# Optimization experiments

Measured on AMD Instinct MI355X. Metric: run time of the kernel, lower is better.

Reference implementation:

```python
import jax, jax.numpy as jnp
import numpy as np

B, N, D = 4, 1024, 1024
H = 16
RS, RC = 32, 32
MLP = int(D * 4.0)
EPS = 1e-6


def _ln(x):
    # LayerNorm with no scale/bias (flax defaults: eps=1e-6)
    m = jnp.mean(x, axis=-1, keepdims=True)
    v = jnp.mean(jnp.square(x - m), axis=-1, keepdims=True)
    return (x - m) * jax.lax.rsqrt(v + EPS)


def _rms(x, scale):
    rms = jnp.sqrt(jnp.mean(jnp.square(x), axis=-1, keepdims=True) + EPS)
    return scale * x / rms


def _modulate(x, shift, scale):
    return x * (1 + scale[:, None]) + shift[:, None]


def setup_inputs() -> dict:
    key = jax.random.key(0)
    ks = jax.random.split(key, 20)
    s = 0.02
    return {
        'x': jax.random.normal(ks[0], (B, N, D), jnp.float32),
        'c': jax.random.normal(ks[1], (B, D), jnp.float32),
        'cls_token': jax.random.normal(ks[2], (B, D), jnp.float32),
        'Wc': jax.random.normal(ks[3], (D, 6 * D), jnp.float32) * s,
        'bc': jax.random.normal(ks[4], (6 * D,), jnp.float32) * s,
        'Wqkv': jax.random.normal(ks[5], (D, 3 * D), jnp.float32) * s,
        'bqkv': jnp.zeros((3 * D,), jnp.float32),
        'Wo': jax.random.normal(ks[6], (D, D), jnp.float32) * s,
        'bo': jnp.zeros((D,), jnp.float32),
        'A_s': jax.random.normal(ks[7], (D, RS), jnp.float32) * s,
        'B_s': jax.random.normal(ks[8], (RS, D), jnp.float32) * s,
        'rms_s_scale': jnp.ones((D,), jnp.float32),
        'C_r': jax.random.normal(ks[9], (D, RC), jnp.float32) * s,
        'D_r': jax.random.normal(ks[10], (RC, D), jnp.float32) * s,
        'rms_c_scale': jnp.ones((D,), jnp.float32),
        'W1': jax.random.normal(ks[11], (D, MLP), jnp.float32) * s,
        'b1': jnp.zeros((MLP,), jnp.float32),
        'W2': jax.random.normal(ks[12], (MLP, D), jnp.float32) * s,
        'b2': jnp.zeros((D,), jnp.float32),
    }


def reference(x, c, cls_token, Wc, bc, Wqkv, bqkv, Wo, bo, A_s, B_s,
              rms_s_scale, C_r, D_r, rms_c_scale, W1, b1, W2, b2):
    hd = D // H
    # AdaLN conditioning
    c_proj = jax.nn.silu(c) @ Wc + bc                    # (B, 6D)
    shift_a, scale_a, gate_a, shift_m, scale_m, gate_m = jnp.split(c_proj, 6, axis=-1)

    # Self-attention branch
    x_norm = _modulate(_ln(x), shift_a, scale_a)         # (B, N, D)
    qkv = x_norm @ Wqkv + bqkv                           # (B, N, 3D)
    q, k, v = jnp.split(qkv, 3, axis=-1)
    q = q.reshape(B, N, H, hd).transpose(0, 2, 1, 3)     # (B, H, N, hd)
    k = k.reshape(B, N, H, hd).transpose(0, 2, 1, 3)
    v = v.reshape(B, N, H, hd).transpose(0, 2, 1, 3)
    attn_w = jax.nn.softmax(jnp.einsum('bhqd,bhkd->bhqk', q, k) * hd ** (-0.5), axis=-1)
    attn_out = jnp.einsum('bhqk,bhkd->bhqd', attn_w, v)
    attn_out = attn_out.transpose(0, 2, 1, 3).reshape(B, N, D)
    attn_out = attn_out @ Wo + bo
    Y = x + gate_a[:, None] * attn_out

    # Self-gram low-rank branch (residual)
    gram_s = (x @ A_s) @ B_s                             # (B, N, D)
    X_prime = _rms(gram_s, rms_s_scale) + Y

    # Cross-gram branch via CLS token (no residual)
    u_c = cls_token[:, :, None] * C_r[None]              # (B, D, RC)
    v_c = jnp.einsum('bnd,bdr->bnr', X_prime, u_c)       # (B, N, RC)
    gram_c = v_c @ D_r                                   # (B, N, D)
    Z = _rms(gram_c, rms_c_scale)

    # MLP branch
    z_norm = _modulate(_ln(Z), shift_m, scale_m)
    h = jax.nn.gelu(z_norm @ W1 + b1) @ W2 + b2
    return Z + gate_m[:, None] * h
```

## Files before the change

### kernel.cpp

```cpp
#include <hip/hip_runtime.h>
#include <stdint.h>

typedef float  f32x4  __attribute__((ext_vector_type(4)));
typedef int    i32x4  __attribute__((ext_vector_type(4)));
typedef __bf16 bf16x4 __attribute__((ext_vector_type(4)));

#define D_    1024
#define SIXD  6144
#define QSCALE 0.18033688011112042f

#define BAR() asm volatile("s_barrier" ::: "memory")

__device__ __forceinline__ void mfma16(const i32x4 &a, const i32x4 &b, f32x4 &c) {
  asm("v_mfma_f32_16x16x32_bf16 %0, %1, %2, %0" : "+v"(c) : "v"(a), "v"(b));
}
__device__ __forceinline__ void mfma16a(const i32x4 &a, const i32x4 &b, f32x4 &c) {
  asm("v_mfma_f32_16x16x32_bf16 %0, %1, %2, %0" : "+a"(c) : "v"(a), "v"(b));
}

__device__ __forceinline__ void gload_lds16(const void* g, void* l) {
  __builtin_amdgcn_global_load_lds(
      (const __attribute__((address_space(1))) uint32_t*)g,
      (__attribute__((address_space(3))) uint32_t*)l, 16, 0, 0);
}

__global__ __launch_bounds__(256)
void cond_gemm(const float* __restrict__ c, const float* __restrict__ Wc,
               const float* __restrict__ bc, float* __restrict__ cproj)
{
  __shared__ float sc[4096];
  __shared__ float tp[8][4][32];
  int tid = threadIdx.x;
  for (int i = tid; i < 4096; i += 256) {
    float v = c[i];
    sc[i] = v / (1.f + __expf(-v));
  }
  __syncthreads();
  int colo = tid & 31, kseg = tid >> 5;
  int col = blockIdx.x * 32 + colo;
  float a0 = 0.f, a1 = 0.f, a2 = 0.f, a3 = 0.f;
  for (int k = kseg * 128; k < kseg * 128 + 128; k++) {
    float w = Wc[(size_t)k * SIXD + col];
    a0 += sc[k] * w; a1 += sc[1024 + k] * w;
    a2 += sc[2048 + k] * w; a3 += sc[3072 + k] * w;
  }
  tp[kseg][0][colo] = a0; tp[kseg][1][colo] = a1;
  tp[kseg][2][colo] = a2; tp[kseg][3][colo] = a3;
  __syncthreads();
  if (kseg == 0) {
#pragma unroll
    for (int b = 0; b < 4; b++) {
      float s = bc[col];
#pragma unroll
      for (int g = 0; g < 8; g++) s += tp[g][b][colo];
      cproj[b * SIXD + col] = s;
    }
  }
}

__global__ __launch_bounds__(256)
void transpose_all(const float* __restrict__ Wqkv, const float* __restrict__ Wo,
                   const float* __restrict__ W1, const float* __restrict__ W2,
                   __bf16* __restrict__ Wqkvt, __bf16* __restrict__ Wot,
                   __bf16* __restrict__ W1t, __bf16* __restrict__ W2t)
{
  __shared__ __bf16 t[64][65];
  int bid = blockIdx.x;
  const float* W; __bf16* Wt; int Kdim, Ndim, lb;
  if (bid < 768)       { W = Wqkv; Wt = Wqkvt; Kdim = 1024; Ndim = 3072; lb = bid; }
  else if (bid < 1024) { W = Wo;   Wt = Wot;   Kdim = 1024; Ndim = 1024; lb = bid - 768; }
  else if (bid < 2048) { W = W1;   Wt = W1t;   Kdim = 1024; Ndim = 4096; lb = bid - 1024; }
  else                 { W = W2;   Wt = W2t;   Kdim = 4096; Ndim = 1024; lb = bid - 2048; }
  int ntn = Ndim >> 6;
  int kt = lb / ntn, nt = lb % ntn;
  int tid = threadIdx.x;
  const float* src = W + (size_t)(kt * 64) * Ndim + nt * 64;
#pragma unroll
  for (int i = 0; i < 4; i++) {
    int k = i * 16 + (tid >> 4);
    int c4 = tid & 15;
    float4 v = ((const float4*)(src + (size_t)k * Ndim))[c4];
    t[k][c4 * 4 + 0] = (__bf16)v.x; t[k][c4 * 4 + 1] = (__bf16)v.y;
    t[k][c4 * 4 + 2] = (__bf16)v.z; t[k][c4 * 4 + 3] = (__bf16)v.w;
  }
  __syncthreads();
  __bf16* dst = Wt + (size_t)(nt * 64) * Kdim + kt * 64;
  int n = tid >> 2, ks = (tid & 3) * 16;
  bf16x4 o0, o1, o2, o3;
#pragma unroll
  for (int j = 0; j < 4; j++) {
    o0[j] = t[ks + j][n];      o1[j] = t[ks + 4 + j][n];
    o2[j] = t[ks + 8 + j][n];  o3[j] = t[ks + 12 + j][n];
  }
  __bf16* dp = dst + (size_t)n * Kdim + ks;
  *(bf16x4*)(dp) = o0; *(bf16x4*)(dp + 4) = o1;
  *(bf16x4*)(dp + 8) = o2; *(bf16x4*)(dp + 12) = o3;
}

__global__ __launch_bounds__(256)
void transpose_v(const __bf16* __restrict__ qkv, __bf16* __restrict__ Vt)
{
  __shared__ __bf16 t[32][33];
  int bid = blockIdx.x;
  int dt = bid & 1, nt = (bid >> 1) & 31, bh = bid >> 6;
  int b = bh >> 4, h = bh & 15;
  int x = threadIdx.x & 31, yq = threadIdx.x >> 5;
  const __bf16* src = qkv + ((size_t)(b * 1024 + nt * 32)) * 3072 + 2048 + h * 64 + dt * 32;
#pragma unroll
  for (int i = 0; i < 4; i++) {
    int row = yq * 4 + i;
    t[row][x] = src[(size_t)row * 3072 + x];
  }
  __syncthreads();
  __bf16* dst = Vt + ((size_t)(bh * 64 + dt * 32)) * 1024 + nt * 32;
#pragma unroll
  for (int i = 0; i < 4; i++) {
    int drow = yq * 4 + i;
    dst[(size_t)drow * 1024 + x] = t[x][drow];
  }
}

__global__ __launch_bounds__(256)
void ln_mod(const float* __restrict__ X, const float* __restrict__ cproj,
            int shift_off, int scale_off, __bf16* __restrict__ Out)
{
  int row = blockIdx.x;
  int b = row >> 10;
  int tid = threadIdx.x;
  const float4* xr = (const float4*)(X + (size_t)row * D_);
  float4 v = xr[tid];
  float s  = v.x + v.y + v.z + v.w;
  float s2 = v.x * v.x + v.y * v.y + v.z * v.z + v.w * v.w;
#pragma unroll
  for (int off = 1; off < 64; off <<= 1) {
    s  += __shfl_xor(s,  off, 64);
    s2 += __shfl_xor(s2, off, 64);
  }
  __shared__ float red[8];
  int wave = tid >> 6, lane = tid & 63;
  if (lane == 0) { red[wave] = s; red[4 + wave] = s2; }
  __syncthreads();
  s  = red[0] + red[1] + red[2] + red[3];
  s2 = red[4] + red[5] + red[6] + red[7];
  float mean = s * (1.f / D_);
  float var  = s2 * (1.f / D_) - mean * mean;
  float rstd = rsqrtf(var + 1e-6f);
  const float4* sh = (const float4*)(cproj + b * SIXD + shift_off);
  const float4* sc = (const float4*)(cproj + b * SIXD + scale_off);
  float4 shv = sh[tid], scv = sc[tid];
  bf16x4 o;
  o[0] = (__bf16)((v.x - mean) * rstd * (1.f + scv.x) + shv.x);
  o[1] = (__bf16)((v.y - mean) * rstd * (1.f + scv.y) + shv.y);
  o[2] = (__bf16)((v.z - mean) * rstd * (1.f + scv.z) + shv.z);
  o[3] = (__bf16)((v.w - mean) * rstd * (1.f + scv.w) + shv.w);
  *(bf16x4*)(Out + (size_t)row * D_ + tid * 4) = o;
}

template<int EPI, int NBUF>
__global__ __launch_bounds__(256)
void gemm_bt(const __bf16* __restrict__ A, const __bf16* __restrict__ Bt,
             const float* __restrict__ bias, const float* __restrict__ cproj,
             int gate_off, const float* __restrict__ resid,
             void* __restrict__ Cout, void* __restrict__ Cout2,
             void* __restrict__ Cout3, void* __restrict__ Cout4,
             int M, int N, int K, int SK)
{
  __shared__ __align__(16) __bf16 As[NBUF * 128 * 32];
  __shared__ __align__(16) __bf16 Bs[NBUF * 128 * 32];
  const int PD = NBUF - 1;
  int tilesN = N >> 7, tilesM = M >> 7;
  int npersk = tilesM * tilesN;
  int sk = blockIdx.x / npersk;
  int rest = blockIdx.x % npersk;
  int cpx = npersk >> 3;
  rest = (rest & 7) * cpx + (rest >> 3);
  int bm = rest / tilesN, bn = rest % tilesN;
  int Klen = K / SK, Kstart = sk * Klen;

  int tid = threadIdx.x;
  int lane = tid & 63, wave = tid >> 6;
  int lr = lane & 15, lg = lane >> 4;
  int wm = (wave >> 1) << 6, wn = (wave & 1) << 6;

  f32x4 acc[4][4] = {};

  int sr = tid >> 2, skb = tid & 3;
  int scol = ((skb ^ ((sr >> 1) & 3)) * 8);
  const __bf16* pa = A + (size_t)((bm << 7) + sr) * K + Kstart + scol;
  const __bf16* pb = Bt + (size_t)((bn << 7) + sr) * K + Kstart + scol;
  const size_t rstep = (size_t)64 * K;
  __bf16* la = As + tid * 8;
  __bf16* lb = Bs + tid * 8;

  auto STAGE = [&](int buf, int k0) {
    int bo = buf * 4096;
    gload_lds16(pa + k0, la + bo);
    gload_lds16(pa + rstep + k0, la + bo + 2048);
    gload_lds16(pb + k0, lb + bo);
    gload_lds16(pb + rstep + k0, lb + bo + 2048);
  };

  int nt = Klen >> 5;
#pragma unroll
  for (int p = 0; p < PD; p++) STAGE(p, p * 32);

  for (int t = 0; t < nt; t++) {
    if (t + PD < nt) STAGE((t + PD) % NBUF, (t + PD) * 32);
    int ahead = nt - 1 - t; if (ahead > PD) ahead = PD;
    if (ahead >= 3)      asm volatile("s_waitcnt vmcnt(12)" ::: "memory");
    else if (ahead == 2) asm volatile("s_waitcnt vmcnt(8)" ::: "memory");
    else if (ahead == 1) asm volatile("s_waitcnt vmcnt(4)" ::: "memory");
    else                 asm volatile("s_waitcnt vmcnt(0)" ::: "memory");
    BAR();
    const __bf16* Ac = As + (t % NBUF) * 4096;
    const __bf16* Bc = Bs + (t % NBUF) * 4096;
    i32x4 af[4], bfv[4];
#pragma unroll
    for (int m = 0; m < 4; m++) {
      int row = wm + m * 16 + lr;
      af[m] = *(const i32x4*)(Ac + row * 32 + ((lg ^ ((row >> 1) & 3)) * 8));
    }
#pragma unroll
    for (int n = 0; n < 4; n++) {
      int row = wn + n * 16 + lr;
      bfv[n] = *(const i32x4*)(Bc + row * 32 + ((lg ^ ((row >> 1) & 3)) * 8));
    }
    asm volatile("s_waitcnt lgkmcnt(0)" ::: "memory");
    __builtin_amdgcn_sched_barrier(0);
    BAR();
    __builtin_amdgcn_s_setprio(1);
#pragma unroll
    for (int m = 0; m < 4; m++)
#pragma unroll
      for (int n = 0; n < 4; n++)
        mfma16(af[m], bfv[n], acc[m][n]);
    __builtin_amdgcn_s_setprio(0);
  }
  asm volatile("s_waitcnt vmcnt(0)" ::: "memory");
  asm volatile("s_nop 7\n\ts_nop 7" ::);

  __bf16* Pp = nullptr;
  if (EPI == 3) {
    if (sk == 0)      Pp = (__bf16*)Cout;
    else if (sk == 1) Pp = (__bf16*)Cout2;
    else if (sk == 2) Pp = (__bf16*)Cout3;
    else              Pp = (__bf16*)Cout4;
  }

  int row0 = (bm << 7) + wm;
  int col0 = (bn << 7) + wn;
#pragma unroll
  for (int m = 0; m < 4; m++) {
#pragma unroll
    for (int n = 0; n < 4; n++) {
      int cc = col0 + n * 16 + lr;
      float bv = (EPI == 3) ? 0.f : bias[cc];
#pragma unroll
      for (int r = 0; r < 4; r++) {
        int row = row0 + m * 16 + (lg << 2) + r;
        float v = acc[m][n][r] + bv;
        size_t idx = (size_t)row * N + cc;
        if (EPI == 0) {
          ((__bf16*)Cout)[idx] = (__bf16)v;
        } else if (EPI == 1) {
          int b = row >> 10;
          float g = cproj[b * SIXD + gate_off + cc];
          ((float*)Cout)[idx] = resid[idx] + g * v;
        } else if (EPI == 2) {
          float u = 0.7978845608028654f * (v + 0.044715f * v * v * v);
          u = fminf(fmaxf(u, -15.f), 15.f);
          float e = __expf(2.f * u);
          float th = (e - 1.f) / (e + 1.f);
          ((__bf16*)Cout)[idx] = (__bf16)(0.5f * v * (1.f + th));
        } else if (EPI == 4) {
          float scq = (cc < 1024) ? QSCALE : 1.f;
          ((__bf16*)Cout)[idx] = (__bf16)(v * scq);
        } else {
          Pp[idx] = (__bf16)v;
        }
      }
    }
  }
}

template<int EPI, int NT, int KD>
__global__ __launch_bounds__(512, 2)
void gemm256(const __bf16* __restrict__ A, const __bf16* __restrict__ Bt,
             const float* __restrict__ bias,
             void* __restrict__ Cout, void* __restrict__ Cout2,
             void* __restrict__ Cout3, void* __restrict__ Cout4,
             int M, int N)
{
  __shared__ __align__(16) __bf16 As[2 * 16384];
  __shared__ __align__(16) __bf16 Bs[2 * 16384];
  int tilesN = N >> 8, tilesM = M >> 8;
  int npersk = tilesM * tilesN;
  int sk = blockIdx.x / npersk;
  int rest = blockIdx.x % npersk;
  int cpx = npersk >> 3;
  rest = (rest & 7) * cpx + (rest >> 3);
  int bm = rest / tilesN, bn = rest % tilesN;
  int Kstart = sk * (NT * 64);

  int tid = threadIdx.x;
  int lane = tid & 63, wave = tid >> 6;
  int lr = lane & 15, lg = lane >> 4;
  int wr = wave >> 2, wc = wave & 3;

  f32x4 acc[8][4] = {};

  int srow = tid >> 3;
  int schunk = (tid & 7) ^ (srow & 7);
  const __bf16* pa = A  + (size_t)((bm << 8) + srow) * KD + Kstart + schunk * 8;
  const __bf16* pb = Bt + (size_t)((bn << 8) + srow) * KD + Kstart + schunk * 8;
  __bf16* la = As + tid * 8;
  __bf16* lb = Bs + tid * 8;

  gload_lds16(pa,                 la);
  gload_lds16(pa + 64 * KD,       la + 4096);
  gload_lds16(pa + 128 * KD,      la + 8192);
  gload_lds16(pa + 192 * KD,      la + 12288);
  gload_lds16(pb,                 lb);
  gload_lds16(pb + 64 * KD,       lb + 4096);
  gload_lds16(pb + 128 * KD,      lb + 8192);
  gload_lds16(pb + 192 * KD,      lb + 12288);
  gload_lds16(pb + 64,            lb + 16384);
  gload_lds16(pb + 64 * KD + 64,  lb + 16384 + 4096);
  gload_lds16(pb + 128 * KD + 64, lb + 16384 + 8192);
  gload_lds16(pb + 192 * KD + 64, lb + 16384 + 12288);
  asm volatile("s_waitcnt vmcnt(4)" ::: "memory");
  BAR();

  int cc0 = ((lg ^ (lr & 7)) << 4);
  int cc1 = cc0 ^ 64;
  const char* aA = (const char*)As + (wr * 128 + lr) * 128;
  const char* aB = (const char*)Bs + (wc * 64 + lr) * 128;

  i32x4 alo[4][2], ahi[4][2], b0v[2][2], b1v[2][2];
#pragma unroll
  for (int m = 0; m < 4; m++) {
    alo[m][0] = *(const i32x4*)(aA + m * 2048 + cc0);
    alo[m][1] = *(const i32x4*)(aA + m * 2048 + cc1);
  }
#pragma unroll
  for (int n = 0; n < 2; n++) {
    b0v[n][0] = *(const i32x4*)(aB + n * 2048 + cc0);
    b0v[n][1] = *(const i32x4*)(aB + n * 2048 + cc1);
  }

  for (int t = 0; t < NT; t++) {
    const char* Ab = aA + (t & 1) * 32768;
    const char* Bb = aB + (t & 1) * 32768;
    int nb = ((t + 1) & 1) * 16384;
    int ob = (t & 1) * 16384;

#pragma unroll
    for (int n = 0; n < 2; n++) {
      b1v[n][0] = *(const i32x4*)(Bb + 4096 + n * 2048 + cc0);
      b1v[n][1] = *(const i32x4*)(Bb + 4096 + n * 2048 + cc1);
    }
    if (t + 1 < NT) {
      gload_lds16(pa + 64,            la + nb);
      gload_lds16(pa + 128 * KD + 64, la + nb + 8192);
    }
    __builtin_amdgcn_s_setprio(1);
#pragma unroll
    for (int m = 0; m < 4; m++)
#pragma unroll
      for (int n = 0; n < 2; n++) {
        mfma16a(alo[m][0], b0v[n][0], acc[m][n]);
        mfma16a(alo[m][1], b0v[n][1], acc[m][n]);
      }
    __builtin_amdgcn_s_setprio(0);
    BAR();

#pragma unroll
    for (int m = 0; m < 4; m++) {
      ahi[m][0] = *(const i32x4*)(Ab + 8192 + m * 2048 + cc0);
      ahi[m][1] = *(const i32x4*)(Ab + 8192 + m * 2048 + cc1);
    }
    if (t + 1 < NT) {
      gload_lds16(pa + 64 * KD + 64,  la + nb + 4096);
      gload_lds16(pa + 192 * KD + 64, la + nb + 12288);
    }
    __builtin_amdgcn_s_setprio(1);
#pragma unroll
    for (int m = 0; m < 4; m++)
#pragma unroll
      for (int n = 0; n < 2; n++) {
        mfma16a(alo[m][0], b1v[n][0], acc[m][2 + n]);
        mfma16a(alo[m][1], b1v[n][1], acc[m][2 + n]);
      }
    __builtin_amdgcn_s_setprio(0);
    BAR();

    if (t + 2 < NT) {
      gload_lds16(pb + 128,           lb + ob);
      gload_lds16(pb + 64 * KD + 128, lb + ob + 4096);
    }
    __builtin_amdgcn_s_setprio(1);
#pragma unroll
    for (int m = 0; m < 4; m++)
#pragma unroll
      for (int n = 0; n < 2; n++) {
        mfma16a(ahi[m][0], b1v[n][0], acc[4 + m][2 + n]);
        mfma16a(ahi[m][1], b1v[n][1], acc[4 + m][2 + n]);
      }
    __builtin_amdgcn_s_setprio(0);
    if (t + 1 < NT) {
      if (t + 2 < NT) asm volatile("s_waitcnt vmcnt(2)" ::: "memory");
      else            asm volatile("s_waitcnt vmcnt(0)" ::: "memory");
    }
    BAR();

    if (t + 2 < NT) {
      gload_lds16(pb + 128 * KD + 128, lb + ob + 8192);
      gload_lds16(pb + 192 * KD + 128, lb + ob + 12288);
    }
    __builtin_amdgcn_s_setprio(1);
#pragma unroll
    for (int m = 0; m < 4; m++)
#pragma unroll
      for (int n = 0; n < 2; n++) {
        mfma16a(ahi[m][0], b0v[n][0], acc[4 + m][n]);
        mfma16a(ahi[m][1], b0v[n][1], acc[4 + m][n]);
      }
    __builtin_amdgcn_s_setprio(0);
    if (t + 1 < NT) {
      const char* An = aA + ((t + 1) & 1) * 32768;
      const char* Bn = aB + ((t + 1) & 1) * 32768;
#pragma unroll
      for (int m = 0; m < 4; m++) {
        alo[m][0] = *(const i32x4*)(An + m * 2048 + cc0);
        alo[m][1] = *(const i32x4*)(An + m * 2048 + cc1);
      }
#pragma unroll
      for (int n = 0; n < 2; n++) {
        b0v[n][0] = *(const i32x4*)(Bn + n * 2048 + cc0);
        b0v[n][1] = *(const i32x4*)(Bn + n * 2048 + cc1);
      }
    }
    BAR();
    pa += 64; pb += 64;
  }
  asm volatile("s_nop 7\n\ts_nop 7" ::);

  __bf16* Pp = nullptr;
  if (EPI == 3) {
    if (sk == 0)      Pp = (__bf16*)Cout;
    else if (sk == 1) Pp = (__bf16*)Cout2;
    else if (sk == 2) Pp = (__bf16*)Cout3;
    else              Pp = (__bf16*)Cout4;
  }

  int row0 = (bm << 8) + wr * 128;
  int col0 = (bn << 8) + wc * 64;
#pragma unroll
  for (int m = 0; m < 8; m++) {
#pragma unroll
    for (int n = 0; n < 4; n++) {
      int cc = col0 + n * 16 + lr;
      float bv = (EPI == 3) ? 0.f : bias[cc];
#pragma unroll
      for (int r = 0; r < 4; r++) {
        int row = row0 + m * 16 + (lg << 2) + r;
        float v = acc[m][n][r] + bv;
        size_t idx = (size_t)row * N + cc;
        if (EPI == 2) {
          float u = 0.7978845608028654f * (v + 0.044715f * v * v * v);
          u = fminf(fmaxf(u, -15.f), 15.f);
          float e = __expf(2.f * u);
          float th = (e - 1.f) / (e + 1.f);
          ((__bf16*)Cout)[idx] = (__bf16)(0.5f * v * (1.f + th));
        } else if (EPI == 4) {
          float scq = (cc < 1024) ? QSCALE : 1.f;
          ((__bf16*)Cout)[idx] = (__bf16)(v * scq);
        } else {
          Pp[idx] = (__bf16)v;
        }
      }
    }
  }
}

__global__ __launch_bounds__(256)
void reduce_w2(const __bf16* __restrict__ P0, const __bf16* __restrict__ P1,
               const __bf16* __restrict__ P2, const __bf16* __restrict__ P3,
               const float* __restrict__ bias, const float* __restrict__ cproj,
               float* __restrict__ Out)
{
  int row = blockIdx.x;
  int b = row >> 10;
  int tid = threadIdx.x;
  size_t base = (size_t)row * D_ + tid * 4;
  bf16x4 a0 = *(const bf16x4*)(P0 + base);
  bf16x4 a1 = *(const bf16x4*)(P1 + base);
  bf16x4 a2 = *(const bf16x4*)(P2 + base);
  bf16x4 a3 = *(const bf16x4*)(P3 + base);
  f32x4 s;
#pragma unroll
  for (int i = 0; i < 4; i++)
    s[i] = ((float)a0[i] + (float)a1[i]) + ((float)a2[i] + (float)a3[i]);
  f32x4 bz = *(const f32x4*)(bias + tid * 4);
  f32x4 g  = *(const f32x4*)(cproj + b * SIXD + 5120 + tid * 4);
  f32x4 z  = *(const f32x4*)(Out + base);
  *(f32x4*)(Out + base) = z + g * (s + bz);
}

__global__ __launch_bounds__(512, 4)
void attn_flash(const __bf16* __restrict__ qkv, const __bf16* __restrict__ Vt,
                __bf16* __restrict__ O)
{
  __shared__ __align__(16) __bf16 Kl[2][64 * 64];
  __shared__ __align__(16) __bf16 Vl[2][64 * 64];
  __shared__ __align__(16) __bf16 Pl[8][16 * 64];

  int bid = ((blockIdx.x & 7) << 6) | (blockIdx.x >> 3);
  int qt = bid & 7, h = (bid >> 3) & 15, b = bid >> 7;
  int tid = threadIdx.x, wave = tid >> 6, lane = tid & 63;
  int lr = lane & 15, lg = lane >> 4;

  size_t tok0 = (size_t)b * 1024;
  int qrow = qt * 128 + wave * 16 + lr;
  const __bf16* qptr = qkv + (tok0 + qrow) * 3072 + h * 64;
  i32x4 qf0 = *(const i32x4*)(qptr + lg * 8);
  i32x4 qf1 = *(const i32x4*)(qptr + 32 + lg * 8);

  float l_acc[4] = {0.f, 0.f, 0.f, 0.f};
  f32x4 oacc[4] = {};

  const __bf16* kbase = qkv + tok0 * 3072 + 1024 + h * 64;
  const __bf16* vbase = Vt + ((size_t)(b * 16 + h) * 64) * 1024;

  int skey = tid >> 3, sdb = tid & 7;
  const __bf16* ksrc = kbase + (size_t)skey * 3072 + ((sdb ^ (skey & 7)) * 8);
  const __bf16* vsrc = vbase + (size_t)skey * 1024 + ((sdb ^ (skey & 7)) * 8);
  __bf16* klp = &Kl[0][0] + tid * 8;
  __bf16* vlp = &Vl[0][0] + tid * 8;
  __bf16* pl = &Pl[wave][0];

  auto STAGE = [&](int buf, int kk) {
    gload_lds16(ksrc + (size_t)kk * 3072, klp + buf * 4096);
    gload_lds16(vsrc + kk, vlp + buf * 4096);
  };

  STAGE(0, 0);
  int cur = 0;
  for (int k0 = 0; k0 < 1024; k0 += 64) {
    int kn = (k0 + 64 < 1024) ? (k0 + 64) : k0;
    STAGE(cur ^ 1, kn);
    asm volatile("s_waitcnt vmcnt(2)" ::: "memory");
    BAR();
    const __bf16* K_ = &Kl[cur][0];
    const __bf16* V_ = &Vl[cur][0];

    f32x4 s[4];
    __builtin_amdgcn_s_setprio(1);
#pragma unroll
    for (int n = 0; n < 4; n++) {
      int key = n * 16 + lr;
      int kx = key & 7;
      i32x4 kf0 = *(const i32x4*)(K_ + key * 64 + ((lg ^ kx) * 8));
      i32x4 kf1 = *(const i32x4*)(K_ + key * 64 + (((4 + lg) ^ kx) * 8));
      f32x4 sa = {0.f, 0.f, 0.f, 0.f};
      mfma16(qf0, kf0, sa);
      mfma16(qf1, kf1, sa);
      s[n] = sa;
    }
    __builtin_amdgcn_s_setprio(0);

#pragma unroll
    for (int n = 0; n < 4; n++)
#pragma unroll
      for (int r = 0; r < 4; r++)
        s[n][r] = exp2f(s[n][r]);
#pragma unroll
    for (int r = 0; r < 4; r++)
      l_acc[r] += (s[0][r] + s[1][r]) + (s[2][r] + s[3][r]);

#pragma unroll
    for (int n = 0; n < 4; n++)
#pragma unroll
      for (int r = 0; r < 4; r++) {
        int prow = lg * 4 + r;
        int key = n * 16 + lr;
        int idx = prow * 64 + (((key >> 3) ^ (prow & 7)) * 8) + (key & 7);
        pl[idx] = (__bf16)s[n][r];
      }
    asm volatile("s_waitcnt lgkmcnt(0)" ::: "memory");
    __builtin_amdgcn_sched_barrier(0);
    i32x4 pf0 = *(const i32x4*)(pl + lr * 64 + ((lg ^ (lr & 7)) * 8));
    i32x4 pf1 = *(const i32x4*)(pl + lr * 64 + (((4 + lg) ^ (lr & 7)) * 8));

    __builtin_amdgcn_s_setprio(1);
#pragma unroll
    for (int dt = 0; dt < 4; dt++) {
      int vrow = dt * 16 + lr, rx = vrow & 7;
      i32x4 vf0 = *(const i32x4*)(V_ + vrow * 64 + ((lg ^ rx) * 8));
      i32x4 vf1 = *(const i32x4*)(V_ + vrow * 64 + (((4 + lg) ^ rx) * 8));
      mfma16(pf0, vf0, oacc[dt]);
      mfma16(pf1, vf1, oacc[dt]);
    }
    __builtin_amdgcn_s_setprio(0);
    asm volatile("s_waitcnt lgkmcnt(0)" ::: "memory");
    __builtin_amdgcn_sched_barrier(0);
    BAR();
    cur ^= 1;
  }
  asm volatile("s_waitcnt vmcnt(0)" ::: "memory");
  asm volatile("s_nop 7\n\ts_nop 7" ::);

  float rinv[4];
#pragma unroll
  for (int r = 0; r < 4; r++) {
    float v = l_acc[r];
#pragma unroll
    for (int off = 1; off < 16; off <<= 1) v += __shfl_xor(v, off, 64);
    rinv[r] = 1.f / v;
  }

  int orow = qt * 128 + wave * 16 + (lg << 2);
#pragma unroll
  for (int dt = 0; dt < 4; dt++)
#pragma unroll
    for (int r = 0; r < 4; r++) {
      float v = oacc[dt][r] * rinv[r];
      O[(tok0 + orow + r) * 1024 + h * 64 + dt * 16 + lr] = (__bf16)v;
    }
}

__global__ __launch_bounds__(256)
void gram_fused(const float* __restrict__ X, const float* __restrict__ Y,
                const float* __restrict__ cls,
                const float* __restrict__ A_s, const float* __restrict__ B_s,
                const float* __restrict__ rms_s,
                const float* __restrict__ C_r, const float* __restrict__ D_r,
                const float* __restrict__ rms_c,
                const float* __restrict__ cproj,
                float* __restrict__ Z, __bf16* __restrict__ Znorm)
{
  __shared__ float xs[4][D_];
  __shared__ float tp[8][4][32];
  __shared__ float t1[4][32];
  __shared__ float red[4][4];
  __shared__ float red2[4][4][2];
  int row0 = blockIdx.x * 4;
  int b = row0 >> 10;
  int tid = threadIdx.x;
  int wv = tid >> 6;

  f32x4 cv = *(const f32x4*)(cls + (size_t)b * D_ + tid * 4);
  f32x4 yv[4];
#pragma unroll
  for (int rr = 0; rr < 4; rr++) {
    ((f32x4*)xs[rr])[tid] = *(const f32x4*)(X + (size_t)(row0 + rr) * D_ + tid * 4);
    yv[rr] = *(const f32x4*)(Y + (size_t)(row0 + rr) * D_ + tid * 4);
  }
  __syncthreads();

  {
    int r = tid & 31, seg = tid >> 5;
    float a0 = 0.f, a1 = 0.f, a2 = 0.f, a3 = 0.f;
    const float* ap = A_s + r;
    for (int d = seg * 128; d < seg * 128 + 128; d++) {
      float w = ap[d * 32];
      a0 += xs[0][d] * w; a1 += xs[1][d] * w;
      a2 += xs[2][d] * w; a3 += xs[3][d] * w;
    }
    tp[seg][0][r] = a0; tp[seg][1][r] = a1; tp[seg][2][r] = a2; tp[seg][3][r] = a3;
  }
  __syncthreads();
  if (tid < 128) {
    int rr = tid >> 5, r = tid & 31;
    float sv = 0.f;
#pragma unroll
    for (int g = 0; g < 8; g++) sv += tp[g][rr][r];
    t1[rr][r] = sv;
  }
  __syncthreads();

  f32x4 g[4] = {};
  for (int r = 0; r < 32; r++) {
    f32x4 bv = *(const f32x4*)(B_s + (size_t)r * D_ + tid * 4);
    g[0] += t1[0][r] * bv; g[1] += t1[1][r] * bv;
    g[2] += t1[2][r] * bv; g[3] += t1[3][r] * bv;
  }
  float ssl[4];
#pragma unroll
  for (int rr = 0; rr < 4; rr++)
    ssl[rr] = g[rr][0]*g[rr][0] + g[rr][1]*g[rr][1] + g[rr][2]*g[rr][2] + g[rr][3]*g[rr][3];
#pragma unroll
  for (int off = 1; off < 64; off <<= 1)
#pragma unroll
    for (int rr = 0; rr < 4; rr++) ssl[rr] += __shfl_xor(ssl[rr], off, 64);
  if ((tid & 63) == 0) {
#pragma unroll
    for (int rr = 0; rr < 4; rr++) red[wv][rr] = ssl[rr];
  }
  __syncthreads();
  {
    f32x4 scv = *(const f32x4*)(rms_s + tid * 4);
#pragma unroll
    for (int rr = 0; rr < 4; rr++) {
      float ss = red[0][rr] + red[1][rr] + red[2][rr] + red[3][rr];
      float rs = rsqrtf(ss * (1.f / D_) + 1e-6f);
      f32x4 xp = scv * g[rr] * rs + yv[rr];
      ((f32x4*)xs[rr])[tid] = xp * cv;
    }
  }
  __syncthreads();

  {
    int r = tid & 31, seg = tid >> 5;
    float a0 = 0.f, a1 = 0.f, a2 = 0.f, a3 = 0.f;
    const float* cp = C_r + r;
    for (int d = seg * 128; d < seg * 128 + 128; d++) {
      float w = cp[d * 32];
      a0 += xs[0][d] * w; a1 += xs[1][d] * w;
      a2 += xs[2][d] * w; a3 += xs[3][d] * w;
    }
    tp[seg][0][r] = a0; tp[seg][1][r] = a1; tp[seg][2][r] = a2; tp[seg][3][r] = a3;
  }
  __syncthreads();
  if (tid < 128) {
    int rr = tid >> 5, r = tid & 31;
    float sv = 0.f;
#pragma unroll
    for (int g2i = 0; g2i < 8; g2i++) sv += tp[g2i][rr][r];
    t1[rr][r] = sv;
  }
  __syncthreads();

  f32x4 g2[4] = {};
  for (int r = 0; r < 32; r++) {
    f32x4 bv = *(const f32x4*)(D_r + (size_t)r * D_ + tid * 4);
    g2[0] += t1[0][r] * bv; g2[1] += t1[1][r] * bv;
    g2[2] += t1[2][r] * bv; g2[3] += t1[3][r] * bv;
  }
#pragma unroll
  for (int rr = 0; rr < 4; rr++)
    ssl[rr] = g2[rr][0]*g2[rr][0] + g2[rr][1]*g2[rr][1] + g2[rr][2]*g2[rr][2] + g2[rr][3]*g2[rr][3];
#pragma unroll
  for (int off = 1; off < 64; off <<= 1)
#pragma unroll
    for (int rr = 0; rr < 4; rr++) ssl[rr] += __shfl_xor(ssl[rr], off, 64);
  if ((tid & 63) == 0) {
#pragma unroll
    for (int rr = 0; rr < 4; rr++) red[wv][rr] = ssl[rr];
  }
  __syncthreads();
  f32x4 z[4];
  {
    f32x4 scv = *(const f32x4*)(rms_c + tid * 4);
#pragma unroll
    for (int rr = 0; rr < 4; rr++) {
      float ss = red[0][rr] + red[1][rr] + red[2][rr] + red[3][rr];
      float rs = rsqrtf(ss * (1.f / D_) + 1e-6f);
      z[rr] = scv * g2[rr] * rs;
    }
  }

  float s1l[4], s2l[4];
#pragma unroll
  for (int rr = 0; rr < 4; rr++) {
    s1l[rr] = z[rr][0] + z[rr][1] + z[rr][2] + z[rr][3];
    s2l[rr] = z[rr][0]*z[rr][0] + z[rr][1]*z[rr][1] + z[rr][2]*z[rr][2] + z[rr][3]*z[rr][3];
  }
#pragma unroll
  for (int off = 1; off < 64; off <<= 1)
#pragma unroll
    for (int rr = 0; rr < 4; rr++) {
      s1l[rr] += __shfl_xor(s1l[rr], off, 64);
      s2l[rr] += __shfl_xor(s2l[rr], off, 64);
    }
  if ((tid & 63) == 0) {
#pragma unroll
    for (int rr = 0; rr < 4; rr++) { red2[wv][rr][0] = s1l[rr]; red2[wv][rr][1] = s2l[rr]; }
  }
  __syncthreads();
  f32x4 shv = *(const f32x4*)(cproj + b * SIXD + 3072 + tid * 4);
  f32x4 scm = *(const f32x4*)(cproj + b * SIXD + 4096 + tid * 4);
#pragma unroll
  for (int rr = 0; rr < 4; rr++) {
    float S  = red2[0][rr][0] + red2[1][rr][0] + red2[2][rr][0] + red2[3][rr][0];
    float S2 = red2[0][rr][1] + red2[1][rr][1] + red2[2][rr][1] + red2[3][rr][1];
    float mean = S * (1.f / D_);
    float var  = S2 * (1.f / D_) - mean * mean;
    float rstd = rsqrtf(var + 1e-6f);
    f32x4 zn = (z[rr] - mean) * rstd * (scm + 1.f) + shv;
    *(f32x4*)(Z + (size_t)(row0 + rr) * D_ + tid * 4) = z[rr];
    bf16x4 o;
#pragma unroll
    for (int i = 0; i < 4; i++) o[i] = (__bf16)zn[i];
    *(bf16x4*)(Znorm + (size_t)(row0 + rr) * D_ + tid * 4) = o;
  }
}

extern "C" void kernel_launch(void* const* d_in, const int* in_sizes, int n_in,
                              void* d_out, int out_size, void* d_ws, size_t ws_size,
                              hipStream_t stream)
{
  const float* x     = (const float*)d_in[0];
  const float* c     = (const float*)d_in[1];
  const float* cls   = (const float*)d_in[2];
  const float* Wc    = (const float*)d_in[3];
  const float* bc    = (const float*)d_in[4];
  const float* Wqkv  = (const float*)d_in[5];
  const float* bqkv  = (const float*)d_in[6];
  const float* Wo    = (const float*)d_in[7];
  const float* bo    = (const float*)d_in[8];
  const float* A_s   = (const float*)d_in[9];
  const float* B_s   = (const float*)d_in[10];
  const float* rms_s = (const float*)d_in[11];
  const float* C_r   = (const float*)d_in[12];
  const float* D_r   = (const float*)d_in[13];
  const float* rms_c = (const float*)d_in[14];
  const float* W1    = (const float*)d_in[15];
  const float* b1    = (const float*)d_in[16];
  const float* W2    = (const float*)d_in[17];
  const float* b2    = (const float*)d_in[18];
  float* out = (float*)d_out;

  float* ws = (float*)d_ws;
  __bf16* Wqkvt = (__bf16*)(ws + 0);
  __bf16* Wot   = (__bf16*)(ws + 1572864);
  __bf16* W1t   = (__bf16*)(ws + 2097152);
  __bf16* W2t   = (__bf16*)(ws + 4194304);
  float*  cproj = ws + 6291456;
  __bf16* xnorm = (__bf16*)(ws + 6316032);
  __bf16* qkv   = (__bf16*)(ws + 8413184);
  __bf16* Vt    = (__bf16*)(ws + 14704640);
  __bf16* h1    = (__bf16*)(ws + 8413184);
  __bf16* attno = (__bf16*)(ws + 16801792);
  float*  Ybuf  = ws + 18898944;
  __bf16* P0 = (__bf16*)(ws + 0);
  __bf16* P1 = (__bf16*)(ws + 2097152);
  __bf16* P2 = (__bf16*)(ws + 16801792);
  __bf16* P3 = (__bf16*)(ws + 18898944);

  cond_gemm<<<192, 256, 0, stream>>>(c, Wc, bc, cproj);
  transpose_all<<<3072, 256, 0, stream>>>(Wqkv, Wo, W1, W2, Wqkvt, Wot, W1t, W2t);
  ln_mod<<<4096, 256, 0, stream>>>(x, cproj, 0, 1024, xnorm);
  gemm256<4, 16, 1024><<<192, 512, 0, stream>>>(xnorm, Wqkvt, bqkv,
                                                qkv, nullptr, nullptr, nullptr,
                                                4096, 3072);
  transpose_v<<<4096, 256, 0, stream>>>(qkv, Vt);
  attn_flash<<<512, 512, 0, stream>>>(qkv, Vt, attno);
  gemm_bt<1, 4><<<256, 256, 0, stream>>>(attno, Wot, bo, cproj, 2048, x,
                                         Ybuf, nullptr, nullptr, nullptr,
                                         4096, 1024, 1024, 1);
  gram_fused<<<1024, 256, 0, stream>>>(x, Ybuf, cls, A_s, B_s, rms_s,
                                       C_r, D_r, rms_c, cproj, out, xnorm);
  gemm256<2, 16, 1024><<<256, 512, 0, stream>>>(xnorm, W1t, b1,
                                                h1, nullptr, nullptr, nullptr,
                                                4096, 4096);
  gemm256<3, 16, 4096><<<256, 512, 0, stream>>>(h1, W2t, nullptr,
                                                P0, P1, P2, P3, 4096, 1024);
  reduce_w2<<<4096, 256, 0, stream>>>(P0, P1, P2, P3, b2, cproj, out);
}
```

Baseline: 267.9 us.

## Prefetch GEMM tiles two K-steps ahead and drop one barrier per iteration

Reworks the bf16 MFMA GEMM main loop so both A and B tiles are fetched two K-steps ahead into the double-buffered LDS, instead of splitting A one step ahead and B two steps ahead. Each buffer is refilled only after its fragments have been read into registers, guarded by explicit lgkmcnt waits. This removes one of the four barriers per iteration. It also adds sched_barriers to keep the compiler from reordering loads across the MFMA blocks. The intent is to hide global-load latency better and cut synchronisation. The cost is more in-flight loads and tighter hazard reasoning about LDS buffer reuse.

```diff
diff --git a/kernel.cpp b/kernel.cpp
--- a/kernel.cpp
+++ b/kernel.cpp
@@ -316,19 +316,24 @@
   __bf16* la = As + tid * 8;
   __bf16* lb = Bs + tid * 8;
 
-  gload_lds16(pa,                 la);
-  gload_lds16(pa + 64 * KD,       la + 4096);
-  gload_lds16(pa + 128 * KD,      la + 8192);
-  gload_lds16(pa + 192 * KD,      la + 12288);
-  gload_lds16(pb,                 lb);
-  gload_lds16(pb + 64 * KD,       lb + 4096);
-  gload_lds16(pb + 128 * KD,      lb + 8192);
-  gload_lds16(pb + 192 * KD,      lb + 12288);
-  gload_lds16(pb + 64,            lb + 16384);
-  gload_lds16(pb + 64 * KD + 64,  lb + 16384 + 4096);
-  gload_lds16(pb + 128 * KD + 64, lb + 16384 + 8192);
-  gload_lds16(pb + 192 * KD + 64, lb + 16384 + 12288);
-  asm volatile("s_waitcnt vmcnt(4)" ::: "memory");
+  auto SAq = [&](int t, int q) {
+    gload_lds16(pa + (size_t)(q * 64) * KD + t * 64,
+                la + (t & 1) * 16384 + q * 4096);
+  };
+  auto SBq = [&](int t, int q) {
+    gload_lds16(pb + (size_t)(q * 64) * KD + t * 64,
+                lb + (t & 1) * 16384 + q * 4096);
+  };
+
+#pragma unroll
+  for (int q = 0; q < 4; q++) { SAq(0, q); }
+#pragma unroll
+  for (int q = 0; q < 4; q++) { SBq(0, q); }
+#pragma unroll
+  for (int q = 0; q < 4; q++) { SAq(1, q); }
+#pragma unroll
+  for (int q = 0; q < 4; q++) { SBq(1, q); }
+  asm volatile("s_waitcnt vmcnt(8)" ::: "memory");
   BAR();
 
   int cc0 = ((lg ^ (lr & 7)) << 4);
@@ -351,18 +356,13 @@
   for (int t = 0; t < NT; t++) {
     const char* Ab = aA + (t & 1) * 32768;
     const char* Bb = aB + (t & 1) * 32768;
-    int nb = ((t + 1) & 1) * 16384;
-    int ob = (t & 1) * 16384;
 
 #pragma unroll
     for (int n = 0; n < 2; n++) {
       b1v[n][0] = *(const i32x4*)(Bb + 4096 + n * 2048 + cc0);
       b1v[n][1] = *(const i32x4*)(Bb + 4096 + n * 2048 + cc1);
     }
-    if (t + 1 < NT) {
-      gload_lds16(pa + 64,            la + nb);
-      gload_lds16(pa + 128 * KD + 64, la + nb + 8192);
-    }
+    __builtin_amdgcn_sched_barrier(0);
     __builtin_amdgcn_s_setprio(1);
 #pragma unroll
     for (int m = 0; m < 4; m++)
@@ -372,6 +372,7 @@
         mfma16a(alo[m][1], b0v[n][1], acc[m][n]);
       }
     __builtin_amdgcn_s_setprio(0);
+    asm volatile("s_waitcnt lgkmcnt(0)" ::: "memory");
     BAR();
 
 #pragma unroll
@@ -379,10 +380,8 @@
       ahi[m][0] = *(const i32x4*)(Ab + 8192 + m * 2048 + cc0);
       ahi[m][1] = *(const i32x4*)(Ab + 8192 + m * 2048 + cc1);
     }
-    if (t + 1 < NT) {
-      gload_lds16(pa + 64 * KD + 64,  la + nb + 4096);
-      gload_lds16(pa + 192 * KD + 64, la + nb + 12288);
-    }
+    if (t + 2 < NT) { SBq(t + 2, 0); SBq(t + 2, 1); }
+    __builtin_amdgcn_sched_barrier(0);
     __builtin_amdgcn_s_setprio(1);
 #pragma unroll
     for (int m = 0; m < 4; m++)
@@ -392,12 +391,14 @@
         mfma16a(alo[m][1], b1v[n][1], acc[m][2 + n]);
       }
     __builtin_amdgcn_s_setprio(0);
+    asm volatile("s_waitcnt lgkmcnt(0)" ::: "memory");
     BAR();
 
     if (t + 2 < NT) {
-      gload_lds16(pb + 128,           lb + ob);
-      gload_lds16(pb + 64 * KD + 128, lb + ob + 4096);
-    }
+      SBq(t + 2, 2); SBq(t + 2, 3);
+      SAq(t + 2, 0); SAq(t + 2, 1); SAq(t + 2, 2); SAq(t + 2, 3);
+    }
+    __builtin_amdgcn_sched_barrier(0);
     __builtin_amdgcn_s_setprio(1);
 #pragma unroll
     for (int m = 0; m < 4; m++)
@@ -406,18 +407,6 @@
         mfma16a(ahi[m][0], b1v[n][0], acc[4 + m][2 + n]);
         mfma16a(ahi[m][1], b1v[n][1], acc[4 + m][2 + n]);
       }
-    __builtin_amdgcn_s_setprio(0);
-    if (t + 1 < NT) {
-      if (t + 2 < NT) asm volatile("s_waitcnt vmcnt(2)" ::: "memory");
-      else            asm volatile("s_waitcnt vmcnt(0)" ::: "memory");
-    }
-    BAR();
-
-    if (t + 2 < NT) {
-      gload_lds16(pb + 128 * KD + 128, lb + ob + 8192);
-      gload_lds16(pb + 192 * KD + 128, lb + ob + 12288);
-    }
-    __builtin_amdgcn_s_setprio(1);
 #pragma unroll
     for (int m = 0; m < 4; m++)
 #pragma unroll
@@ -427,6 +416,9 @@
       }
     __builtin_amdgcn_s_setprio(0);
     if (t + 1 < NT) {
+      if (t + 2 < NT) asm volatile("s_waitcnt vmcnt(8)" ::: "memory");
+      else            asm volatile("s_waitcnt vmcnt(0)" ::: "memory");
+      BAR();
       const char* An = aA + ((t + 1) & 1) * 32768;
       const char* Bn = aB + ((t + 1) & 1) * 32768;
 #pragma unroll
@@ -440,9 +432,8 @@
         b0v[n][1] = *(const i32x4*)(Bn + n * 2048 + cc1);
       }
     }
-    BAR();
-    pa += 64; pb += 64;
-  }
+  }
+  asm volatile("s_waitcnt lgkmcnt(0)" ::: "memory");
   asm volatile("s_nop 7\n\ts_nop 7" ::);
 
   __bf16* Pp = nullptr;
```

New measurement: 265.1 us. No clear change (-1.0%).
